# Kernel optimization log

Measured on AMD Instinct MI355X. Metric: run time of the kernel, lower is better.

## Reference

```python
import jax, jax.numpy as jnp
import numpy as np
from jax import lax

# ---- static hyperparams (match init_kwargs) ----
N_WINDOW = 1024
FRAME_SIZE = 960
C_CONTENT = 192
C_SPK = 256
C_INT = 512
KSIZE = 7
N_LAYERS = 6
MLP_MUL = 3
B = 8
N_FRAMES = 512
L = N_FRAMES * FRAME_SIZE  # 491520
D_MLP = C_INT * MLP_MUL


def _ln_channel(x, g, b, eps=1e-6):
    # channel-wise LayerNorm on (B, C, T): normalize over C per (b, t)
    mu = jnp.mean(x, axis=1, keepdims=True)
    var = jnp.var(x, axis=1, keepdims=True)
    return (x - mu) * lax.rsqrt(var + eps) * g[None, :, None] + b[None, :, None]


def setup_inputs() -> dict:
    key = jax.random.key(0)
    ks = jax.random.split(key, 16)
    s = 0.02
    return {
        "content": jax.random.normal(ks[0], (B, C_CONTENT, N_FRAMES), jnp.float32),
        "f0": jax.random.uniform(ks[1], (B, 1, N_FRAMES), jnp.float32) * 400.0,
        "energy": jax.random.normal(ks[2], (B, 1, N_FRAMES), jnp.float32),
        "spk": jax.random.normal(ks[3], (B, C_SPK, 1), jnp.float32),
        "source": jax.random.normal(ks[4], (B, 1, L), jnp.float32),
        # 1x1 input convs (stored as matrices)
        "w_content": jax.random.normal(ks[5], (C_INT, C_CONTENT), jnp.float32) * s,
        "b_content": jnp.zeros((C_INT,), jnp.float32),
        "w_spk": jax.random.normal(ks[6], (C_INT, C_SPK), jnp.float32) * s,
        "b_spk": jnp.zeros((C_INT,), jnp.float32),
        "w_f0": jax.random.normal(ks[7], (C_INT,), jnp.float32) * s,
        "b_f0": jnp.zeros((C_INT,), jnp.float32),
        "w_energy": jax.random.normal(ks[8], (C_INT,), jnp.float32) * s,
        "b_energy": jnp.zeros((C_INT,), jnp.float32),
        # ConvNeXt layers (stacked over N_LAYERS)
        "dw_w": jax.random.normal(ks[9], (N_LAYERS, C_INT, KSIZE), jnp.float32) * s,
        "dw_b": jnp.zeros((N_LAYERS, C_INT), jnp.float32),
        "ln_g": jnp.ones((N_LAYERS, C_INT), jnp.float32),
        "ln_b": jnp.zeros((N_LAYERS, C_INT), jnp.float32),
        "pw1_w": jax.random.normal(ks[10], (N_LAYERS, D_MLP, C_INT), jnp.float32) * s,
        "pw1_b": jnp.zeros((N_LAYERS, D_MLP), jnp.float32),
        "pw2_w": jax.random.normal(ks[11], (N_LAYERS, C_INT, D_MLP), jnp.float32) * s,
        "pw2_b": jnp.zeros((N_LAYERS, C_INT), jnp.float32),
        # output norm + filter head (Conv1d(C_INT, n_window, 7, pad=3, replicate))
        "out_ln_g": jnp.ones((C_INT,), jnp.float32),
        "out_ln_b": jnp.zeros((C_INT,), jnp.float32),
        "w_out": jax.random.normal(ks[12], (N_WINDOW, C_INT, KSIZE), jnp.float32) * s,
        "b_out": jnp.zeros((N_WINDOW,), jnp.float32),
    }


def reference(content, f0, energy, spk, source,
              w_content, b_content, w_spk, b_spk, w_f0, b_f0, w_energy, b_energy,
              dw_w, dw_b, ln_g, ln_b, pw1_w, pw1_b, pw2_w, pw2_b,
              out_ln_g, out_ln_b, w_out, b_out):
    # --- conditioning trunk ---
    x = jnp.einsum('oc,bct->bot', w_content, content) + b_content[None, :, None]
    x = x + jnp.einsum('oc,bct->bot', w_spk, spk) + b_spk[None, :, None]  # broadcast over T
    logf0 = jnp.log(jax.nn.relu(f0) + 1e-6)  # (B,1,T)
    x = x + w_f0[None, :, None] * logf0 + b_f0[None, :, None]
    x = x + w_energy[None, :, None] * energy + b_energy[None, :, None]

    # --- ConvNeXt stack ---
    for i in range(N_LAYERS):
        res = x
        h = lax.conv_general_dilated(
            x, dw_w[i][:, None, :], (1,), [(KSIZE // 2, KSIZE // 2)],
            dimension_numbers=('NCH', 'OIH', 'NCH'), feature_group_count=C_INT)
        h = h + dw_b[i][None, :, None]
        h = _ln_channel(h, ln_g[i], ln_b[i])
        h = jnp.einsum('oc,bct->bot', pw1_w[i], h) + pw1_b[i][None, :, None]
        h = jax.nn.gelu(h, approximate=False)
        h = jnp.einsum('oc,bct->bot', pw2_w[i], h) + pw2_b[i][None, :, None]
        x = res + h

    x = _ln_channel(x, out_ln_g, out_ln_b)

    # --- filter head: Conv1d k=7 pad=3 replicate ---
    xp = jnp.pad(x, ((0, 0), (0, 0), (KSIZE // 2, KSIZE // 2)), mode='edge')
    filt = lax.conv_general_dilated(
        xp, w_out, (1,), 'VALID', dimension_numbers=('NCH', 'OIH', 'NCH'))
    filt = filt + b_out[None, :, None]           # (B, n_window, T)
    filt = jnp.transpose(filt, (0, 2, 1))        # (B, N_FRAMES, n_window)

    # --- per-frame time-varying FIR: grouped conv, one filter per (b, frame) ---
    frames = source.reshape(B, N_FRAMES, FRAME_SIZE)
    frames = jnp.pad(frames, ((0, 0), (0, 0), (N_WINDOW, N_WINDOW - 1)))  # len 3007
    BN = B * N_FRAMES
    lhs = frames.reshape(1, BN, FRAME_SIZE + 2 * N_WINDOW - 1)
    rhs = filt.reshape(BN, 1, N_WINDOW)
    conv = lax.conv_general_dilated(
        lhs, rhs, (1,), 'VALID', dimension_numbers=('NCH', 'OIH', 'NCH'),
        feature_group_count=BN)                  # (1, BN, FRAME_SIZE + N_WINDOW)
    win = FRAME_SIZE + N_WINDOW                  # 1984
    conv = conv.reshape(B, N_FRAMES, win)

    # --- overlap-add fold (stride FRAME_SIZE) ---
    out_len = L + N_WINDOW
    idx = (jnp.arange(N_FRAMES)[:, None] * FRAME_SIZE
           + jnp.arange(win)[None, :]).reshape(-1)
    out = jnp.zeros((B, out_len), conv.dtype).at[:, idx].add(conv.reshape(B, -1))
    return out[:, None, :L]                      # (B, 1, L)
```

## Files before the change

kernel.cpp:

```cpp
#include <hip/hip_runtime.h>
#include <math.h>

#define NB 8
#define NT 512
#define NROWS 4096
#define CI 512
#define DM 1536
#define CCON 192
#define CSPK 256
#define NW 1024
#define FS 960
#define LTOT 491520
#define CONVW 1984

typedef __bf16 bf16x8 __attribute__((ext_vector_type(8)));
typedef float f32x4 __attribute__((ext_vector_type(4)));
typedef unsigned short ushort;
typedef unsigned int uint;

__device__ __forceinline__ ushort f2bf(float x) {
    union { float f; unsigned u; } v; v.f = x;
    unsigned r = v.u + 0x7fff + ((v.u >> 16) & 1);
    return (ushort)(r >> 16);
}

#define ASYNC_COPY16(g, l) __builtin_amdgcn_global_load_lds( \
    (const __attribute__((address_space(1))) void*)(g), \
    (__attribute__((address_space(3))) void*)(l), 16, 0, 0)

__global__ void cvt_bf16(const float* __restrict__ in, ushort* __restrict__ out, int n4) {
    int i = blockIdx.x * 256 + threadIdx.x;
    if (i < n4) {
        float4 v = ((const float4*)in)[i];
        ushort4 o; o.x = f2bf(v.x); o.y = f2bf(v.y); o.z = f2bf(v.z); o.w = f2bf(v.w);
        ((ushort4*)out)[i] = o;
    }
}

__global__ void cvt_wout(const float* __restrict__ w, ushort* __restrict__ wk) {
    int n = blockIdx.x, tid = threadIdx.x;
    __shared__ ushort s[7][512];
#pragma unroll
    for (int h = 0; h < 2; ++h) {
        int c = tid + h * 256;
        const float* p = w + ((size_t)n * 512 + c) * 7;
#pragma unroll
        for (int k = 0; k < 7; ++k) s[k][c] = f2bf(p[k]);
    }
    __syncthreads();
#pragma unroll
    for (int k = 0; k < 7; ++k)
#pragma unroll
        for (int h = 0; h < 2; ++h) {
            int c = tid + h * 256;
            wk[((size_t)k * NW + n) * CI + c] = s[k][c];
        }
}

__global__ void spkbase_kernel(const float* __restrict__ spk, const float* __restrict__ w_spk,
                               const float* __restrict__ b_spk, const float* __restrict__ b_content,
                               const float* __restrict__ b_f0, const float* __restrict__ b_energy,
                               float* __restrict__ base) {
    int b = blockIdx.x, tid = threadIdx.x;
    __shared__ float s[CSPK];
    if (tid < CSPK) s[tid] = spk[b * CSPK + tid];
    __syncthreads();
    for (int o = tid; o < CI; o += 256) {
        float acc = 0.f;
        for (int c = 0; c < CSPK; ++c) acc = fmaf(w_spk[o * CSPK + c], s[c], acc);
        base[b * CI + o] = acc + b_spk[o] + b_content[o] + b_f0[o] + b_energy[o];
    }
}

__global__ void transpose_content(const float* __restrict__ content, ushort* __restrict__ ct) {
    __shared__ float tile[32][33];
    int b = blockIdx.z, c0 = blockIdx.y * 32, t0 = blockIdx.x * 32;
    int x = threadIdx.x, y = threadIdx.y;
#pragma unroll
    for (int i = 0; i < 32; i += 8)
        tile[y + i][x] = content[((size_t)b * CCON + c0 + y + i) * NT + t0 + x];
    __syncthreads();
#pragma unroll
    for (int i = 0; i < 32; i += 8)
        ct[((size_t)b * NT + t0 + y + i) * CCON + c0 + x] = f2bf(tile[x][y + i]);
}

template <int MODE>
__global__ __launch_bounds__(256) void gemm_mfma64(
    const ushort* __restrict__ A, const ushort* __restrict__ W,
    const float* __restrict__ bias, void* __restrict__ outp,
    const float* __restrict__ res, int K, int NC,
    const float* __restrict__ f0, const float* __restrict__ energy,
    const float* __restrict__ w_f0, const float* __restrict__ w_energy,
    const float* __restrict__ base) {
    __shared__ ushort As[64 * 32];
    __shared__ ushort Bs[64 * 32];
    int tid = threadIdx.x;
    int wave = tid >> 6, lane = tid & 63;
    int m0 = blockIdx.x * 64, n0 = blockIdx.y * 64;
    int srow = tid >> 2, schunk = tid & 3;
    int sg = schunk ^ ((srow >> 1) & 3);
    const ushort* Ag = A + (size_t)(m0 + srow) * K + sg * 8;
    const ushort* Wg = W + (size_t)(n0 + srow) * K + sg * 8;
    const int ldst = srow * 32 + schunk * 8;
    int lm = lane & 15, kq = lane >> 4;
    int csw = (kq ^ ((lm >> 1) & 3)) * 8;
    int wm = wave & 1, wn = wave >> 1;
    f32x4 acc[2][2];
#pragma unroll
    for (int i = 0; i < 2; ++i)
#pragma unroll
        for (int j = 0; j < 2; ++j) acc[i][j] = (f32x4)0.f;

    for (int k0 = 0; k0 < K; k0 += 32) {
        ASYNC_COPY16(Ag + k0, &As[ldst]);
        ASYNC_COPY16(Wg + k0, &Bs[ldst]);
        __syncthreads();
        bf16x8 af[2], bf[2];
#pragma unroll
        for (int i = 0; i < 2; ++i)
            af[i] = *(const bf16x8*)&As[(wm * 32 + i * 16 + lm) * 32 + csw];
#pragma unroll
        for (int j = 0; j < 2; ++j)
            bf[j] = *(const bf16x8*)&Bs[(wn * 32 + j * 16 + lm) * 32 + csw];
#pragma unroll
        for (int i = 0; i < 2; ++i)
#pragma unroll
            for (int j = 0; j < 2; ++j)
                acc[i][j] = __builtin_amdgcn_mfma_f32_16x16x32_bf16(af[i], bf[j], acc[i][j], 0, 0, 0);
        __syncthreads();
    }

    int colv[2];
#pragma unroll
    for (int j = 0; j < 2; ++j) colv[j] = n0 + wn * 32 + j * 16 + lm;
    float p0[2], p1[2], p2[2];
#pragma unroll
    for (int j = 0; j < 2; ++j) {
        if (MODE == 0) {
            int bb = m0 >> 9;
            p0[j] = base[(bb << 9) + colv[j]];
            p1[j] = w_f0[colv[j]];
            p2[j] = w_energy[colv[j]];
        } else {
            p0[j] = bias[colv[j]];
        }
    }
#pragma unroll
    for (int i = 0; i < 2; ++i)
#pragma unroll
        for (int r = 0; r < 4; ++r) {
            int row = m0 + wm * 32 + i * 16 + kq * 4 + r;
            float fv = 0.f, ev = 0.f;
            if (MODE == 0) {
                fv = logf(fmaxf(f0[row], 0.f) + 1e-6f);
                ev = energy[row];
            }
#pragma unroll
            for (int j = 0; j < 2; ++j) {
                float v = acc[i][j][r];
                if (MODE == 0) {
                    v += p0[j] + p1[j] * fv + p2[j] * ev;
                    ((float*)outp)[(size_t)row * NC + colv[j]] = v;
                } else if (MODE == 1) {
                    v += p0[j];
                    v = 0.5f * v * (1.f + erff(v * 0.70710678118654752f));
                    ((ushort*)outp)[(size_t)row * NC + colv[j]] = f2bf(v);
                } else {
                    v += p0[j] + res[(size_t)row * NC + colv[j]];
                    ((float*)outp)[(size_t)row * NC + colv[j]] = v;
                }
            }
        }
}

__global__ __launch_bounds__(256) void head_mfma(
    const ushort* __restrict__ H, const ushort* __restrict__ WK,
    const float* __restrict__ bias, ushort* __restrict__ out) {
    __shared__ ushort As[64 * 32];
    __shared__ ushort Bs[64 * 32];
    int tid = threadIdx.x;
    int wave = tid >> 6, lane = tid & 63;
    int m0 = blockIdx.x * 64, n0 = blockIdx.y * 64;
    int b = m0 >> 9, tbase = m0 & (NT - 1);
    int srow = tid >> 2, schunk = tid & 3;
    int sg = schunk ^ ((srow >> 1) & 3);
    const int ldst = srow * 32 + schunk * 8;
    int lm = lane & 15, kq = lane >> 4;
    int csw = (kq ^ ((lm >> 1) & 3)) * 8;
    int wm = wave & 1, wn = wave >> 1;
    f32x4 acc[2][2];
#pragma unroll
    for (int i = 0; i < 2; ++i)
#pragma unroll
        for (int j = 0; j < 2; ++j) acc[i][j] = (f32x4)0.f;

    for (int k = 0; k < 7; ++k) {
        int t = tbase + srow + k - 3;
        t = min(max(t, 0), NT - 1);
        const ushort* Ag = H + ((size_t)(b << 9) + t) * CI + sg * 8;
        const ushort* Wg = WK + ((size_t)k * NW + n0 + srow) * CI + sg * 8;
        for (int c0 = 0; c0 < CI; c0 += 32) {
            ASYNC_COPY16(Ag + c0, &As[ldst]);
            ASYNC_COPY16(Wg + c0, &Bs[ldst]);
            __syncthreads();
            bf16x8 af[2], bf[2];
#pragma unroll
            for (int i = 0; i < 2; ++i)
                af[i] = *(const bf16x8*)&As[(wm * 32 + i * 16 + lm) * 32 + csw];
#pragma unroll
            for (int j = 0; j < 2; ++j)
                bf[j] = *(const bf16x8*)&Bs[(wn * 32 + j * 16 + lm) * 32 + csw];
#pragma unroll
            for (int i = 0; i < 2; ++i)
#pragma unroll
                for (int j = 0; j < 2; ++j)
                    acc[i][j] = __builtin_amdgcn_mfma_f32_16x16x32_bf16(af[i], bf[j], acc[i][j], 0, 0, 0);
            __syncthreads();
        }
    }
#pragma unroll
    for (int i = 0; i < 2; ++i)
#pragma unroll
        for (int j = 0; j < 2; ++j) {
            int col = n0 + wn * 32 + j * 16 + lm;
            float bv = bias[col];
#pragma unroll
            for (int r = 0; r < 4; ++r) {
                int row = m0 + wm * 32 + i * 16 + kq * 4 + r;
                out[(size_t)row * NW + col] = f2bf(acc[i][j][r] + bv);
            }
        }
}

template <bool DW>
__global__ __launch_bounds__(256) void dwln_kernel(const float* __restrict__ X, ushort* __restrict__ H,
                                                   const float* __restrict__ dw_w,
                                                   const float* __restrict__ dw_b,
                                                   const float* __restrict__ g,
                                                   const float* __restrict__ bb) {
    __shared__ float wt[7][512];
    int tid = threadIdx.x;
    if (DW) {
        for (int i = tid; i < 3584; i += 256) {
            int c = i / 7, k = i - c * 7;
            wt[k][c] = dw_w[i];
        }
        __syncthreads();
    }
    int wid = tid >> 6, lane = tid & 63;
    int n = blockIdx.x * 4 + wid;
    int b = n >> 9, t = n & (NT - 1);
    float v[8];
    if (DW) {
#pragma unroll
        for (int i = 0; i < 8; ++i) v[i] = dw_b[lane + 64 * i];
#pragma unroll
        for (int k = 0; k < 7; ++k) {
            int tt = t + k - 3;
            if (tt >= 0 && tt < NT) {
                const float* xr = X + ((size_t)(b << 9) + tt) * CI + lane;
#pragma unroll
                for (int i = 0; i < 8; ++i)
                    v[i] = fmaf(wt[k][lane + 64 * i], xr[64 * i], v[i]);
            }
        }
    } else {
        const float* xr = X + (size_t)n * CI + lane;
#pragma unroll
        for (int i = 0; i < 8; ++i) v[i] = xr[64 * i];
    }
    float s1 = 0.f, s2 = 0.f;
#pragma unroll
    for (int i = 0; i < 8; ++i) { s1 += v[i]; s2 = fmaf(v[i], v[i], s2); }
#pragma unroll
    for (int off = 1; off < 64; off <<= 1) {
        s1 += __shfl_xor(s1, off);
        s2 += __shfl_xor(s2, off);
    }
    float mean = s1 * (1.f / CI);
    float rs = rsqrtf(s2 * (1.f / CI) - mean * mean + 1e-6f);
    ushort* hr = H + (size_t)n * CI + lane;
#pragma unroll
    for (int i = 0; i < 8; ++i) {
        int c = lane + 64 * i;
        hr[64 * i] = f2bf((v[i] - mean) * rs * g[c] + bb[c]);
    }
}

__global__ __launch_bounds__(256) void fir_mfma(const float* __restrict__ source,
                                                const ushort* __restrict__ filt,
                                                float* __restrict__ conv) {
    __shared__ ushort sp[3088];
    __shared__ uint Bcm32[16 * 532];
    uint* sp32 = (uint*)sp;
    uint* G = sp32 + 1004;
    int tid = threadIdx.x;
    int bg = blockIdx.x;
    int b = bg >> 9, g = bg & (NT - 1);

    for (int i = tid; i < 520; i += 256) sp32[i] = 0;
    if (tid < 16) G[tid] = 0;
    else if (tid < 24) G[512 + tid] = 0;
    const uint* fr32 = (const uint*)(filt + (size_t)bg * NW);
    G[16 + tid] = fr32[tid];
    G[272 + tid] = fr32[256 + tid];
    if (tid < 240) {
        float4 sv = ((const float4*)(source + (size_t)b * LTOT + g * FS))[tid];
        ushort4 o; o.x = f2bf(sv.x); o.y = f2bf(sv.y); o.z = f2bf(sv.z); o.w = f2bf(sv.w);
        *(ushort4*)&sp[1040 + tid * 4] = o;
    }
    __syncthreads();

#pragma unroll 1
    for (int p = 0; p < 3; ++p) {
        int d = tid + p * 256;
        if (d < 528) {
            uint w[9];
#pragma unroll
            for (int q = 0; q < 9; ++q) w[q] = G[d + q];
#pragma unroll
            for (int ul = 0; ul < 16; ++ul) {
                uint val;
                if ((ul & 1) == 0) val = w[8 - (ul >> 1)];
                else {
                    int a = 8 - ((ul + 1) >> 1);
                    val = (w[a] >> 16) | (w[a + 1] << 16);
                }
                Bcm32[ul * 532 + d] = val;
            }
        }
    }
    __syncthreads();

    for (int i = 1000 + tid; i < 1544; i += 256) sp32[i] = 0;
    __syncthreads();

    int wave = tid >> 6, lane = tid & 63;
    int ln = lane & 15, kq = lane >> 4;
    const ushort* Abase = &sp[16 * ln + 8 * kq];
    const ushort* Bbase = (const ushort*)&Bcm32[ln * 532] + 8 * kq;
    int mt0 = wave * 2;
    f32x4 acc0 = (f32x4)0.f, acc1 = (f32x4)0.f;
#pragma unroll 3
    for (int kt = 0; kt < 33; ++kt) {
        bf16x8 bfrag = *(const bf16x8*)(Bbase + 32 * kt);
        bf16x8 a0 = *(const bf16x8*)(Abase + 256 * mt0 + 32 * kt);
        bf16x8 a1 = *(const bf16x8*)(Abase + 256 * (mt0 + 1) + 32 * kt);
        acc0 = __builtin_amdgcn_mfma_f32_16x16x32_bf16(a0, bfrag, acc0, 0, 0, 0);
        acc1 = __builtin_amdgcn_mfma_f32_16x16x32_bf16(a1, bfrag, acc1, 0, 0, 0);
    }
    float* cv = conv + (size_t)bg * CONVW;
#pragma unroll
    for (int r = 0; r < 4; ++r) {
        int m0 = mt0 * 16 + kq * 4 + r;
        cv[16 * m0 + ln] = acc0[r];
        int m1 = m0 + 16;
        if (m1 < 124) cv[16 * m1 + ln] = acc1[r];
    }
}

__global__ void fold_kernel(const float* __restrict__ conv, float* __restrict__ out) {
    int b = blockIdx.y;
    int t = blockIdx.x * blockDim.x + threadIdx.x;
    float sum = 0.f;
    int G = (t - 1) / 960;
#pragma unroll
    for (int r = 0; r < 3; ++r) {
        int g = G - r;
        if (g >= 0) {
            int u = t - 960 * g;
            if (u < CONVW) sum += conv[((size_t)(b * NT + g)) * CONVW + u];
        }
    }
    out[(size_t)b * LTOT + t] = sum;
}

extern "C" void kernel_launch(void* const* d_in, const int* in_sizes, int n_in,
                              void* d_out, int out_size, void* d_ws, size_t ws_size,
                              hipStream_t stream) {
    const float* content  = (const float*)d_in[0];
    const float* f0       = (const float*)d_in[1];
    const float* energy   = (const float*)d_in[2];
    const float* spk      = (const float*)d_in[3];
    const float* source   = (const float*)d_in[4];
    const float* w_content= (const float*)d_in[5];
    const float* b_content= (const float*)d_in[6];
    const float* w_spk    = (const float*)d_in[7];
    const float* b_spk    = (const float*)d_in[8];
    const float* w_f0     = (const float*)d_in[9];
    const float* b_f0     = (const float*)d_in[10];
    const float* w_energy = (const float*)d_in[11];
    const float* b_energy = (const float*)d_in[12];
    const float* dw_w     = (const float*)d_in[13];
    const float* dw_b     = (const float*)d_in[14];
    const float* ln_g     = (const float*)d_in[15];
    const float* ln_b     = (const float*)d_in[16];
    const float* pw1_w    = (const float*)d_in[17];
    const float* pw1_b    = (const float*)d_in[18];
    const float* pw2_w    = (const float*)d_in[19];
    const float* pw2_b    = (const float*)d_in[20];
    const float* out_ln_g = (const float*)d_in[21];
    const float* out_ln_b = (const float*)d_in[22];
    const float* w_out    = (const float*)d_in[23];
    const float* b_out    = (const float*)d_in[24];
    float* out = (float*)d_out;

    float* ws = (float*)d_ws;
    float*  x     = ws;
    float*  base  = ws + 2097152;
    ushort* ctb   = (ushort*)(ws + 2101248);
    ushort* wcb   = (ushort*)(ws + 2494464);
    ushort* filtb = (ushort*)(ws + 2543616);
    ushort* h     = (ushort*)(ws + 4640768);
    ushort* pw1w  = (ushort*)(ws + 5689344);
    ushort* pw2w  = (ushort*)(ws + 8048640);
    ushort* wk    = (ushort*)(ws + 10407936);
    ushort* hmid  = (ushort*)(ws + 12242944);
    float*  conv  = ws + 5689344;

    cvt_bf16<<<4608, 256, 0, stream>>>(pw1_w, pw1w, 1179648);
    cvt_bf16<<<4608, 256, 0, stream>>>(pw2_w, pw2w, 1179648);
    cvt_bf16<<<96, 256, 0, stream>>>(w_content, wcb, 24576);
    cvt_wout<<<NW, 256, 0, stream>>>(w_out, wk);
    spkbase_kernel<<<NB, 256, 0, stream>>>(spk, w_spk, b_spk, b_content, b_f0, b_energy, base);
    transpose_content<<<dim3(16, 6, NB), dim3(32, 8), 0, stream>>>(content, ctb);

    gemm_mfma64<0><<<dim3(NROWS / 64, CI / 64), 256, 0, stream>>>(
        ctb, wcb, nullptr, x, nullptr, CCON, CI, f0, energy, w_f0, w_energy, base);

    for (int i = 0; i < 6; ++i) {
        dwln_kernel<true><<<NROWS / 4, 256, 0, stream>>>(x, h, dw_w + i * CI * 7, dw_b + i * CI,
                                                         ln_g + i * CI, ln_b + i * CI);
        gemm_mfma64<1><<<dim3(NROWS / 64, DM / 64), 256, 0, stream>>>(
            h, pw1w + (size_t)i * DM * CI, pw1_b + i * DM, hmid, nullptr, CI, DM,
            nullptr, nullptr, nullptr, nullptr, nullptr);
        gemm_mfma64<2><<<dim3(NROWS / 64, CI / 64), 256, 0, stream>>>(
            hmid, pw2w + (size_t)i * CI * DM, pw2_b + i * CI, x, x, DM, CI,
            nullptr, nullptr, nullptr, nullptr, nullptr);
    }

    dwln_kernel<false><<<NROWS / 4, 256, 0, stream>>>(x, h, nullptr, nullptr, out_ln_g, out_ln_b);
    head_mfma<<<dim3(NROWS / 64, NW / 64), 256, 0, stream>>>(h, wk, b_out, filtb);
    fir_mfma<<<NROWS, 256, 0, stream>>>(source, filtb, conv);
    fold_kernel<<<dim3(LTOT / 256, NB), 256, 0, stream>>>(conv, out);
}
```

Measured before the change: 552.2 us.

## Load GEMM operands directly from global into registers and widen N tile

The GEMM and head kernels no longer stage A and W tiles through LDS with async copies and barriers. Each wave now loads its MFMA fragments straight from global memory into registers, and the per-block N tile grows from 64 to 128 so each wave computes a 32x64 output. This removes LDS traffic and the barriers, at the cost of redundant global and L2 reads across waves and less coalesced 16-byte strided loads. The grid is halved along N.

```diff
diff --git a/kernel.cpp b/kernel.cpp
--- a/kernel.cpp
+++ b/kernel.cpp
@@ -24,10 +24,6 @@
     return (ushort)(r >> 16);
 }
 
-#define ASYNC_COPY16(g, l) __builtin_amdgcn_global_load_lds( \
-    (const __attribute__((address_space(1))) void*)(g), \
-    (__attribute__((address_space(3))) void*)(l), 16, 0, 0)
-
 __global__ void cvt_bf16(const float* __restrict__ in, ushort* __restrict__ out, int n4) {
     int i = blockIdx.x * 256 + threadIdx.x;
     if (i < n4) {
@@ -86,57 +82,48 @@
 }
 
 template <int MODE>
-__global__ __launch_bounds__(256) void gemm_mfma64(
+__global__ __launch_bounds__(256) void gemm_reg(
     const ushort* __restrict__ A, const ushort* __restrict__ W,
     const float* __restrict__ bias, void* __restrict__ outp,
     const float* __restrict__ res, int K, int NC,
     const float* __restrict__ f0, const float* __restrict__ energy,
     const float* __restrict__ w_f0, const float* __restrict__ w_energy,
     const float* __restrict__ base) {
-    __shared__ ushort As[64 * 32];
-    __shared__ ushort Bs[64 * 32];
     int tid = threadIdx.x;
     int wave = tid >> 6, lane = tid & 63;
-    int m0 = blockIdx.x * 64, n0 = blockIdx.y * 64;
-    int srow = tid >> 2, schunk = tid & 3;
-    int sg = schunk ^ ((srow >> 1) & 3);
-    const ushort* Ag = A + (size_t)(m0 + srow) * K + sg * 8;
-    const ushort* Wg = W + (size_t)(n0 + srow) * K + sg * 8;
-    const int ldst = srow * 32 + schunk * 8;
     int lm = lane & 15, kq = lane >> 4;
-    int csw = (kq ^ ((lm >> 1) & 3)) * 8;
     int wm = wave & 1, wn = wave >> 1;
-    f32x4 acc[2][2];
+    int m0 = blockIdx.x * 64, n0 = blockIdx.y * 128;
+    const ushort* Ap = A + (size_t)(m0 + wm * 32 + lm) * K + kq * 8;
+    const ushort* Wp = W + (size_t)(n0 + wn * 64 + lm) * K + kq * 8;
+    f32x4 acc[2][4];
 #pragma unroll
     for (int i = 0; i < 2; ++i)
 #pragma unroll
-        for (int j = 0; j < 2; ++j) acc[i][j] = (f32x4)0.f;
-
+        for (int j = 0; j < 4; ++j) acc[i][j] = (f32x4)0.f;
+
+#pragma unroll 2
     for (int k0 = 0; k0 < K; k0 += 32) {
-        ASYNC_COPY16(Ag + k0, &As[ldst]);
-        ASYNC_COPY16(Wg + k0, &Bs[ldst]);
-        __syncthreads();
-        bf16x8 af[2], bf[2];
+        bf16x8 af[2], bf[4];
 #pragma unroll
         for (int i = 0; i < 2; ++i)
-            af[i] = *(const bf16x8*)&As[(wm * 32 + i * 16 + lm) * 32 + csw];
-#pragma unroll
-        for (int j = 0; j < 2; ++j)
-            bf[j] = *(const bf16x8*)&Bs[(wn * 32 + j * 16 + lm) * 32 + csw];
+            af[i] = *(const bf16x8*)(Ap + (size_t)i * 16 * K + k0);
+#pragma unroll
+        for (int j = 0; j < 4; ++j)
+            bf[j] = *(const bf16x8*)(Wp + (size_t)j * 16 * K + k0);
 #pragma unroll
         for (int i = 0; i < 2; ++i)
 #pragma unroll
-            for (int j = 0; j < 2; ++j)
+            for (int j = 0; j < 4; ++j)
                 acc[i][j] = __builtin_amdgcn_mfma_f32_16x16x32_bf16(af[i], bf[j], acc[i][j], 0, 0, 0);
-        __syncthreads();
-    }
-
-    int colv[2];
-#pragma unroll
-    for (int j = 0; j < 2; ++j) colv[j] = n0 + wn * 32 + j * 16 + lm;
-    float p0[2], p1[2], p2[2];
-#pragma unroll
-    for (int j = 0; j < 2; ++j) {
+    }
+
+    int colv[4];
+#pragma unroll
+    for (int j = 0; j < 4; ++j) colv[j] = n0 + wn * 64 + j * 16 + lm;
+    float p0[4], p1[4], p2[4];
+#pragma unroll
+    for (int j = 0; j < 4; ++j) {
         if (MODE == 0) {
             int bb = m0 >> 9;
             p0[j] = base[(bb << 9) + colv[j]];
@@ -157,7 +144,7 @@
                 ev = energy[row];
             }
 #pragma unroll
-            for (int j = 0; j < 2; ++j) {
+            for (int j = 0; j < 4; ++j) {
                 float v = acc[i][j][r];
                 if (MODE == 0) {
                     v += p0[j] + p1[j] * fv + p2[j] * ev;
@@ -174,56 +161,51 @@
         }
 }
 
-__global__ __launch_bounds__(256) void head_mfma(
+__global__ __launch_bounds__(256) void head_reg(
     const ushort* __restrict__ H, const ushort* __restrict__ WK,
     const float* __restrict__ bias, ushort* __restrict__ out) {
-    __shared__ ushort As[64 * 32];
-    __shared__ ushort Bs[64 * 32];
     int tid = threadIdx.x;
     int wave = tid >> 6, lane = tid & 63;
-    int m0 = blockIdx.x * 64, n0 = blockIdx.y * 64;
+    int lm = lane & 15, kq = lane >> 4;
+    int wm = wave & 1, wn = wave >> 1;
+    int m0 = blockIdx.x * 64, n0 = blockIdx.y * 128;
     int b = m0 >> 9, tbase = m0 & (NT - 1);
-    int srow = tid >> 2, schunk = tid & 3;
-    int sg = schunk ^ ((srow >> 1) & 3);
-    const int ldst = srow * 32 + schunk * 8;
-    int lm = lane & 15, kq = lane >> 4;
-    int csw = (kq ^ ((lm >> 1) & 3)) * 8;
-    int wm = wave & 1, wn = wave >> 1;
-    f32x4 acc[2][2];
+    f32x4 acc[2][4];
 #pragma unroll
     for (int i = 0; i < 2; ++i)
 #pragma unroll
-        for (int j = 0; j < 2; ++j) acc[i][j] = (f32x4)0.f;
+        for (int j = 0; j < 4; ++j) acc[i][j] = (f32x4)0.f;
 
     for (int k = 0; k < 7; ++k) {
-        int t = tbase + srow + k - 3;
-        t = min(max(t, 0), NT - 1);
-        const ushort* Ag = H + ((size_t)(b << 9) + t) * CI + sg * 8;
-        const ushort* Wg = WK + ((size_t)k * NW + n0 + srow) * CI + sg * 8;
+        const ushort* ap[2];
+#pragma unroll
+        for (int i = 0; i < 2; ++i) {
+            int t = tbase + wm * 32 + i * 16 + lm + k - 3;
+            t = min(max(t, 0), NT - 1);
+            ap[i] = H + ((size_t)(b << 9) + t) * CI + kq * 8;
+        }
+        const ushort* wp = WK + ((size_t)k * NW + n0 + wn * 64 + lm) * CI + kq * 8;
+#pragma unroll 2
         for (int c0 = 0; c0 < CI; c0 += 32) {
-            ASYNC_COPY16(Ag + c0, &As[ldst]);
-            ASYNC_COPY16(Wg + c0, &Bs[ldst]);
-            __syncthreads();
-            bf16x8 af[2], bf[2];
+            bf16x8 af[2], bf[4];
 #pragma unroll
             for (int i = 0; i < 2; ++i)
-                af[i] = *(const bf16x8*)&As[(wm * 32 + i * 16 + lm) * 32 + csw];
-#pragma unroll
-            for (int j = 0; j < 2; ++j)
-                bf[j] = *(const bf16x8*)&Bs[(wn * 32 + j * 16 + lm) * 32 + csw];
+                af[i] = *(const bf16x8*)(ap[i] + c0);
+#pragma unroll
+            for (int j = 0; j < 4; ++j)
+                bf[j] = *(const bf16x8*)(wp + (size_t)j * 16 * CI + c0);
 #pragma unroll
             for (int i = 0; i < 2; ++i)
 #pragma unroll
-                for (int j = 0; j < 2; ++j)
+                for (int j = 0; j < 4; ++j)
                     acc[i][j] = __builtin_amdgcn_mfma_f32_16x16x32_bf16(af[i], bf[j], acc[i][j], 0, 0, 0);
-            __syncthreads();
         }
     }
 #pragma unroll
     for (int i = 0; i < 2; ++i)
 #pragma unroll
-        for (int j = 0; j < 2; ++j) {
-            int col = n0 + wn * 32 + j * 16 + lm;
+        for (int j = 0; j < 4; ++j) {
+            int col = n0 + wn * 64 + j * 16 + lm;
             float bv = bias[col];
 #pragma unroll
             for (int r = 0; r < 4; ++r) {
@@ -426,22 +408,22 @@
     spkbase_kernel<<<NB, 256, 0, stream>>>(spk, w_spk, b_spk, b_content, b_f0, b_energy, base);
     transpose_content<<<dim3(16, 6, NB), dim3(32, 8), 0, stream>>>(content, ctb);
 
-    gemm_mfma64<0><<<dim3(NROWS / 64, CI / 64), 256, 0, stream>>>(
+    gemm_reg<0><<<dim3(NROWS / 64, CI / 128), 256, 0, stream>>>(
         ctb, wcb, nullptr, x, nullptr, CCON, CI, f0, energy, w_f0, w_energy, base);
 
     for (int i = 0; i < 6; ++i) {
         dwln_kernel<true><<<NROWS / 4, 256, 0, stream>>>(x, h, dw_w + i * CI * 7, dw_b + i * CI,
                                                          ln_g + i * CI, ln_b + i * CI);
-        gemm_mfma64<1><<<dim3(NROWS / 64, DM / 64), 256, 0, stream>>>(
+        gemm_reg<1><<<dim3(NROWS / 64, DM / 128), 256, 0, stream>>>(
             h, pw1w + (size_t)i * DM * CI, pw1_b + i * DM, hmid, nullptr, CI, DM,
             nullptr, nullptr, nullptr, nullptr, nullptr);
-        gemm_mfma64<2><<<dim3(NROWS / 64, CI / 64), 256, 0, stream>>>(
+        gemm_reg<2><<<dim3(NROWS / 64, CI / 128), 256, 0, stream>>>(
             hmid, pw2w + (size_t)i * CI * DM, pw2_b + i * CI, x, x, DM, CI,
             nullptr, nullptr, nullptr, nullptr, nullptr);
     }
 
     dwln_kernel<false><<<NROWS / 4, 256, 0, stream>>>(x, h, nullptr, nullptr, out_ln_g, out_ln_b);
-    head_mfma<<<dim3(NROWS / 64, NW / 64), 256, 0, stream>>>(h, wk, b_out, filtb);
+    head_reg<<<dim3(NROWS / 64, NW / 128), 256, 0, stream>>>(h, wk, b_out, filtb);
     fir_mfma<<<NROWS, 256, 0, stream>>>(source, filtb, conv);
     fold_kernel<<<dim3(LTOT / 256, NB), 256, 0, stream>>>(conv, out);
 }
```

Measured after the change: 883.1 us. +59.9%, slower.
